# Performance work log

Hardware: AMD Instinct MI355X
Metric: run time of the kernel (lower is better)

## Reference

```python
import jax, jax.numpy as jnp
import numpy as np

N = 100000
E = 1600000
D_IN = 64
D_H = 64
D_OUT = 10
EPS_BN = 1e-5
EPS_NORM = 1e-12


def setup_inputs() -> dict:
    key = jax.random.key(0)
    ks = jax.random.split(key, 16)
    x = jax.random.normal(ks[0], (N, D_IN), dtype=jnp.float32)
    edge_index = jax.random.randint(ks[1], (2, E), 0, N, dtype=jnp.int64)
    def lin(k, fo, fi):
        s = 1.0 / np.sqrt(fi)
        return jax.random.uniform(k, (fo, fi), jnp.float32, -s, s)
    return {
        "x": x, "edge_index": edge_index,
        "Wl1": lin(ks[2], D_H, D_IN), "Wr1": lin(ks[3], D_H, D_IN), "b1": jnp.zeros((D_H,), jnp.float32),
        "g1": jnp.ones((D_H,), jnp.float32), "be1": jnp.zeros((D_H,), jnp.float32),
        "Wl2": lin(ks[4], D_H, D_H), "Wr2": lin(ks[5], D_H, D_H), "b2": jnp.zeros((D_H,), jnp.float32),
        "g2": jnp.ones((D_H,), jnp.float32), "be2": jnp.zeros((D_H,), jnp.float32),
        "Wl3": lin(ks[6], D_OUT, D_H), "Wr3": lin(ks[7], D_OUT, D_H), "b3": jnp.zeros((D_OUT,), jnp.float32),
    }


def _sage_conv(x, src, dst, Wl, Wr, b, normalize):
    # mean aggregation over incoming edges (messages flow src -> dst)
    agg = jax.ops.segment_sum(x[src], dst, num_segments=N)
    cnt = jax.ops.segment_sum(jnp.ones((src.shape[0],), x.dtype), dst, num_segments=N)
    mean = agg / jnp.clip(cnt, 1.0)[:, None]
    out = mean @ Wl.T + x @ Wr.T + b
    if normalize:
        nrm = jnp.sqrt(jnp.sum(out * out, axis=-1, keepdims=True))
        out = out / jnp.maximum(nrm, EPS_NORM)
    return out


def _batchnorm(x, gamma, beta):
    mu = jnp.mean(x, axis=0)
    var = jnp.mean((x - mu) ** 2, axis=0)  # biased var (training mode)
    return (x - mu) * jax.lax.rsqrt(var + EPS_BN) * gamma + beta


def reference(x, edge_index, Wl1, Wr1, b1, g1, be1, Wl2, Wr2, b2, g2, be2, Wl3, Wr3, b3):
    src, dst = edge_index[0], edge_index[1]
    h = _sage_conv(x, src, dst, Wl1, Wr1, b1, True)
    h = jax.nn.relu(_batchnorm(h, g1, be1))
    h = _sage_conv(h, src, dst, Wl2, Wr2, b2, True)
    h = jax.nn.relu(_batchnorm(h, g2, be2))
    h = _sage_conv(h, src, dst, Wl3, Wr3, b3, False)
    return h
```

## Files before the change

kernel.cpp:

```cpp
#include <hip/hip_runtime.h>
#include <hip/hip_bf16.h>

#define NN 100000
#define EE 1600000
#define BSZ 512
#define NBKT 196
#define CHUNK 8192
#define NCH 196

typedef short bf16x8 __attribute__((ext_vector_type(8)));
typedef float f32x4 __attribute__((ext_vector_type(4)));

__device__ inline unsigned short bf16_of(float f) {
    __hip_bfloat16 h = __float2bfloat16(f);
    return *reinterpret_cast<unsigned short*>(&h);
}
__device__ inline unsigned pack2(float a, float b) {
    return (unsigned)bf16_of(a) | ((unsigned)bf16_of(b) << 16);
}
__device__ inline float bflo(unsigned u) { return __uint_as_float(u << 16); }
__device__ inline float bfhi(unsigned u) { return __uint_as_float(u & 0xffff0000u); }


__global__ __launch_bounds__(256)
void k_ccount(const int* __restrict__ ei, int* __restrict__ ccount) {
    __shared__ int hist[NBKT];
    int tid = threadIdx.x;
    int e0 = blockIdx.x * CHUNK;
    int e1 = e0 + CHUNK; if (e1 > EE) e1 = EE;
    for (int i = tid; i < NBKT; i += 256) hist[i] = 0;
    __syncthreads();
    for (int e = e0 + tid; e < e1; e += 256)
        atomicAdd(&hist[ei[EE + e] >> 9], 1);
    __syncthreads();
    for (int i = tid; i < NBKT; i += 256)
        if (hist[i]) atomicAdd(&ccount[i], hist[i]);
}

__global__ void k_cscan(const int* __restrict__ ccount, int* __restrict__ cbase,
                        int* __restrict__ gcur) {
    __shared__ int s[256];
    int tid = threadIdx.x;
    int v = (tid < NBKT) ? ccount[tid] : 0;
    s[tid] = v;
    __syncthreads();
    for (int off = 1; off < 256; off <<= 1) {
        int t = (tid >= off) ? s[tid - off] : 0;
        __syncthreads();
        if (tid >= off) s[tid] += t;
        __syncthreads();
    }
    if (tid < NBKT) {
        int excl = s[tid] - v;
        cbase[tid] = excl;
        gcur[tid] = excl;
    }
    if (tid == NBKT - 1) cbase[NBKT] = s[tid];
}

__global__ __launch_bounds__(256)
void k_coarse(const int* __restrict__ ei, int* __restrict__ gcur, int2* __restrict__ pairs) {
    __shared__ int hist[NBKT];
    __shared__ int base[NBKT];
    __shared__ int curs[NBKT];
    int tid = threadIdx.x;
    int e0 = blockIdx.x * CHUNK;
    int e1 = e0 + CHUNK; if (e1 > EE) e1 = EE;
    for (int i = tid; i < NBKT; i += 256) hist[i] = 0;
    __syncthreads();
    for (int e = e0 + tid; e < e1; e += 256)
        atomicAdd(&hist[ei[EE + e] >> 9], 1);
    __syncthreads();
    for (int i = tid; i < NBKT; i += 256) {
        base[i] = atomicAdd(&gcur[i], hist[i]);
        curs[i] = 0;
    }
    __syncthreads();
    for (int e = e0 + tid; e < e1; e += 256) {
        int src = ei[e];
        int dst = ei[EE + e];
        int b = dst >> 9;
        int off = atomicAdd(&curs[b], 1);
        pairs[base[b] + off] = make_int2(src, dst);
    }
}

__global__ __launch_bounds__(512)
void k_fine(const int* __restrict__ cbase, const int2* __restrict__ pairs,
            int* __restrict__ rs, int* __restrict__ esrc) {
    __shared__ int deg[BSZ];
    __shared__ int s[BSZ];
    int b = blockIdx.x;
    int n0 = b * BSZ;
    int nlocal = NN - n0; if (nlocal > BSZ) nlocal = BSZ;
    int tid = threadIdx.x;
    deg[tid] = 0;
    __syncthreads();
    int e0 = cbase[b], e1 = cbase[b + 1];
    for (int e = e0 + tid; e < e1; e += 512)
        atomicAdd(&deg[pairs[e].y - n0], 1);
    __syncthreads();
    int v = deg[tid];
    s[tid] = v;
    __syncthreads();
    for (int off = 1; off < 512; off <<= 1) {
        int t = (tid >= off) ? s[tid - off] : 0;
        __syncthreads();
        if (tid >= off) s[tid] += t;
        __syncthreads();
    }
    int excl = s[tid] - v;
    if (tid < nlocal) rs[n0 + tid] = e0 + excl;
    if (b == NBKT - 1 && tid == 0) rs[NN] = EE;
    deg[tid] = e0 + excl;
    __syncthreads();
    for (int e = e0 + tid; e < e1; e += 512) {
        int2 p = pairs[e];
        int pos = atomicAdd(&deg[p.y - n0], 1);
        esrc[pos] = p.x;
    }
}

__global__ void k_tobf(const float4* __restrict__ src, ushort4* __restrict__ dst) {
    int i = blockIdx.x * 256 + threadIdx.x;
    if (i >= NN * 16) return;
    float4 v = src[i];
    dst[i] = make_ushort4(bf16_of(v.x), bf16_of(v.y), bf16_of(v.z), bf16_of(v.w));
}

__global__ void k_packW(const float* __restrict__ Wl1, const float* __restrict__ Wr1,
                        const float* __restrict__ Wl2, const float* __restrict__ Wr2,
                        unsigned short* __restrict__ w1, unsigned short* __restrict__ w2) {
    int tid = threadIdx.x;
    for (int i = tid; i < 8192; i += 256) {
        int n = i >> 7, k = i & 127;
        float v1 = (k < 64) ? Wl1[n * 64 + k] : Wr1[n * 64 + (k - 64)];
        w1[i] = bf16_of(v1);
        float v2 = (k < 64) ? Wl2[n * 64 + k] : Wr2[n * 64 + (k - 64)];
        w2[i] = bf16_of(v2);
    }
}

__global__ __launch_bounds__(256)
void k_aggbf(const unsigned short* __restrict__ xbf, const int* __restrict__ rs,
             const int* __restrict__ esrc, unsigned short* __restrict__ meanbf,
             const float* __restrict__ sc, const float* __restrict__ sh) {
    int gid = blockIdx.x * 256 + threadIdx.x;
    int node = gid >> 6;
    if (node >= NN) return;
    int lane = threadIdx.x & 63;
    int c = lane & 7;
    int slot = lane >> 3;
    int s0 = rs[node], s1 = rs[node + 1];
    const uint4* xb = (const uint4*)xbf;
    float a0 = 0.f, a1 = 0.f, a2 = 0.f, a3 = 0.f, a4 = 0.f, a5 = 0.f, a6 = 0.f, a7 = 0.f;
    if (sc) {
        float4 scl = ((const float4*)sc)[2 * c], sch = ((const float4*)sc)[2 * c + 1];
        float4 shl = ((const float4*)sh)[2 * c], shh = ((const float4*)sh)[2 * c + 1];
        for (int p = s0 + slot; p < s1; p += 8) {
            uint4 v = xb[esrc[p] * 8 + c];
            a0 += fmaxf(fmaf(bflo(v.x), scl.x, shl.x), 0.f);
            a1 += fmaxf(fmaf(bfhi(v.x), scl.y, shl.y), 0.f);
            a2 += fmaxf(fmaf(bflo(v.y), scl.z, shl.z), 0.f);
            a3 += fmaxf(fmaf(bfhi(v.y), scl.w, shl.w), 0.f);
            a4 += fmaxf(fmaf(bflo(v.z), sch.x, shh.x), 0.f);
            a5 += fmaxf(fmaf(bfhi(v.z), sch.y, shh.y), 0.f);
            a6 += fmaxf(fmaf(bflo(v.w), sch.z, shh.z), 0.f);
            a7 += fmaxf(fmaf(bfhi(v.w), sch.w, shh.w), 0.f);
        }
    } else {
        for (int p = s0 + slot; p < s1; p += 8) {
            uint4 v = xb[esrc[p] * 8 + c];
            a0 += bflo(v.x); a1 += bfhi(v.x);
            a2 += bflo(v.y); a3 += bfhi(v.y);
            a4 += bflo(v.z); a5 += bfhi(v.z);
            a6 += bflo(v.w); a7 += bfhi(v.w);
        }
    }
#pragma unroll
    for (int m = 8; m <= 32; m <<= 1) {
        a0 += __shfl_xor(a0, m, 64); a1 += __shfl_xor(a1, m, 64);
        a2 += __shfl_xor(a2, m, 64); a3 += __shfl_xor(a3, m, 64);
        a4 += __shfl_xor(a4, m, 64); a5 += __shfl_xor(a5, m, 64);
        a6 += __shfl_xor(a6, m, 64); a7 += __shfl_xor(a7, m, 64);
    }
    if (slot == 0) {
        int cnt = s1 - s0; if (cnt < 1) cnt = 1;
        float inv = 1.0f / (float)cnt;
        uint4 o;
        o.x = pack2(a0 * inv, a1 * inv);
        o.y = pack2(a2 * inv, a3 * inv);
        o.z = pack2(a4 * inv, a5 * inv);
        o.w = pack2(a6 * inv, a7 * inv);
        ((uint4*)meanbf)[node * 8 + c] = o;
    }
}

__global__ __launch_bounds__(256, 4)
void k_sagemfma(const unsigned short* __restrict__ meanbf,
                const unsigned short* __restrict__ a2bf,
                const unsigned short* __restrict__ Wbf,
                const float* __restrict__ bias,
                unsigned short* __restrict__ outbf,
                float* __restrict__ partials,
                const float* __restrict__ sc, const float* __restrict__ sh) {
    __shared__ float sblk[64];
    __shared__ float qblk[64];
    const int tid = threadIdx.x;
    const int base = blockIdx.x * 64;
    const int col = tid & 15;
    const int q   = (tid >> 4) & 3;
    const int w   = tid >> 6;

    if (tid < 64) { sblk[tid] = 0.f; qblk[tid] = 0.f; }

    int gn = base + w * 16 + col; if (gn > NN - 1) gn = NN - 1;
    const uint4* mb = (const uint4*)meanbf;
    const uint4* ab = (const uint4*)a2bf;
    const uint4* wb = (const uint4*)Wbf;

    uint4 fa0 = mb[gn * 8 + q];
    uint4 fa1 = mb[gn * 8 + 4 + q];
    uint4 fa2 = ab[gn * 8 + q];
    uint4 fa3 = ab[gn * 8 + 4 + q];
    if (sc) {
        float4 s0 = ((const float4*)sc)[q * 2],     s1 = ((const float4*)sc)[q * 2 + 1];
        float4 h0 = ((const float4*)sh)[q * 2],     h1 = ((const float4*)sh)[q * 2 + 1];
        float4 s2 = ((const float4*)sc)[8 + q * 2], s3 = ((const float4*)sc)[8 + q * 2 + 1];
        float4 h2 = ((const float4*)sh)[8 + q * 2], h3 = ((const float4*)sh)[8 + q * 2 + 1];
        fa2.x = pack2(fmaxf(fmaf(bflo(fa2.x), s0.x, h0.x), 0.f),
                      fmaxf(fmaf(bfhi(fa2.x), s0.y, h0.y), 0.f));
        fa2.y = pack2(fmaxf(fmaf(bflo(fa2.y), s0.z, h0.z), 0.f),
                      fmaxf(fmaf(bfhi(fa2.y), s0.w, h0.w), 0.f));
        fa2.z = pack2(fmaxf(fmaf(bflo(fa2.z), s1.x, h1.x), 0.f),
                      fmaxf(fmaf(bfhi(fa2.z), s1.y, h1.y), 0.f));
        fa2.w = pack2(fmaxf(fmaf(bflo(fa2.w), s1.z, h1.z), 0.f),
                      fmaxf(fmaf(bfhi(fa2.w), s1.w, h1.w), 0.f));
        fa3.x = pack2(fmaxf(fmaf(bflo(fa3.x), s2.x, h2.x), 0.f),
                      fmaxf(fmaf(bfhi(fa3.x), s2.y, h2.y), 0.f));
        fa3.y = pack2(fmaxf(fmaf(bflo(fa3.y), s2.z, h2.z), 0.f),
                      fmaxf(fmaf(bfhi(fa3.y), s2.w, h2.w), 0.f));
        fa3.z = pack2(fmaxf(fmaf(bflo(fa3.z), s3.x, h3.x), 0.f),
                      fmaxf(fmaf(bfhi(fa3.z), s3.y, h3.y), 0.f));
        fa3.w = pack2(fmaxf(fmaf(bflo(fa3.w), s3.z, h3.z), 0.f),
                      fmaxf(fmaf(bfhi(fa3.w), s3.w, h3.w), 0.f));
    }
    uint4 fa[4] = {fa0, fa1, fa2, fa3};

    f32x4 acc0 = {0.f, 0.f, 0.f, 0.f}, acc1 = acc0, acc2 = acc0, acc3 = acc0;
#pragma unroll
    for (int c = 0; c < 4; ++c) {
        uint4 b0 = wb[(0 * 16 + col) * 16 + c * 4 + q];
        uint4 b1 = wb[(1 * 16 + col) * 16 + c * 4 + q];
        uint4 b2 = wb[(2 * 16 + col) * 16 + c * 4 + q];
        uint4 b3 = wb[(3 * 16 + col) * 16 + c * 4 + q];
        bf16x8 a = *(const bf16x8*)&fa[c];
        acc0 = __builtin_amdgcn_mfma_f32_16x16x32_bf16(a, *(const bf16x8*)&b0, acc0, 0, 0, 0);
        acc1 = __builtin_amdgcn_mfma_f32_16x16x32_bf16(a, *(const bf16x8*)&b1, acc1, 0, 0, 0);
        acc2 = __builtin_amdgcn_mfma_f32_16x16x32_bf16(a, *(const bf16x8*)&b2, acc2, 0, 0, 0);
        acc3 = __builtin_amdgcn_mfma_f32_16x16x32_bf16(a, *(const bf16x8*)&b3, acc3, 0, 0, 0);
    }

    float bb0 = bias[col], bb1 = bias[16 + col], bb2 = bias[32 + col], bb3 = bias[48 + col];
    float sj0 = 0.f, sj1 = 0.f, sj2 = 0.f, sj3 = 0.f;
    float qj0 = 0.f, qj1 = 0.f, qj2 = 0.f, qj3 = 0.f;
#pragma unroll
    for (int r = 0; r < 4; ++r) {
        int go = base + w * 16 + q * 4 + r;
        float o0 = acc0[r] + bb0, o1 = acc1[r] + bb1;
        float o2 = acc2[r] + bb2, o3 = acc3[r] + bb3;
        float ssv = o0 * o0 + o1 * o1 + o2 * o2 + o3 * o3;
        ssv += __shfl_xor(ssv, 1, 64);
        ssv += __shfl_xor(ssv, 2, 64);
        ssv += __shfl_xor(ssv, 4, 64);
        ssv += __shfl_xor(ssv, 8, 64);
        float inv = 1.0f / fmaxf(sqrtf(ssv), 1e-12f);
        o0 *= inv; o1 *= inv; o2 *= inv; o3 *= inv;
        if (go < NN) {
            outbf[go * 64 + col]      = bf16_of(o0);
            outbf[go * 64 + 16 + col] = bf16_of(o1);
            outbf[go * 64 + 32 + col] = bf16_of(o2);
            outbf[go * 64 + 48 + col] = bf16_of(o3);
            sj0 += o0; sj1 += o1; sj2 += o2; sj3 += o3;
            qj0 += o0 * o0; qj1 += o1 * o1; qj2 += o2 * o2; qj3 += o3 * o3;
        }
    }
#pragma unroll
    for (int m = 16; m <= 32; m <<= 1) {
        sj0 += __shfl_xor(sj0, m, 64); sj1 += __shfl_xor(sj1, m, 64);
        sj2 += __shfl_xor(sj2, m, 64); sj3 += __shfl_xor(sj3, m, 64);
        qj0 += __shfl_xor(qj0, m, 64); qj1 += __shfl_xor(qj1, m, 64);
        qj2 += __shfl_xor(qj2, m, 64); qj3 += __shfl_xor(qj3, m, 64);
    }
    __syncthreads();
    if (q == 0) {
        atomicAdd(&sblk[col], sj0);      atomicAdd(&qblk[col], qj0);
        atomicAdd(&sblk[16 + col], sj1); atomicAdd(&qblk[16 + col], qj1);
        atomicAdd(&sblk[32 + col], sj2); atomicAdd(&qblk[32 + col], qj2);
        atomicAdd(&sblk[48 + col], sj3); atomicAdd(&qblk[48 + col], qj3);
    }
    __syncthreads();
    if (tid < 128)
        partials[blockIdx.x * 128 + tid] = (tid < 64) ? sblk[tid] : qblk[tid - 64];
}

__global__ __launch_bounds__(256)
void k_bnred(const float* __restrict__ partials, int nblk, float* __restrict__ red) {
    __shared__ float s[256];
    int tid = threadIdx.x;
    int idx = tid & 127, half = tid >> 7;
    float a0 = 0.f, a1 = 0.f, a2 = 0.f, a3 = 0.f;
    int r = blockIdx.x * 2 + half;
    for (; r + 192 < nblk; r += 256) {
        a0 += partials[r * 128 + idx];
        a1 += partials[(r + 64) * 128 + idx];
        a2 += partials[(r + 128) * 128 + idx];
        a3 += partials[(r + 192) * 128 + idx];
    }
    for (; r < nblk; r += 64) a0 += partials[r * 128 + idx];
    s[tid] = (a0 + a1) + (a2 + a3);
    __syncthreads();
    if (tid < 128) red[blockIdx.x * 128 + tid] = s[tid] + s[tid + 128];
}

__global__ void k_bnfin(const float* __restrict__ red,
                        const float* __restrict__ g, const float* __restrict__ be,
                        float* __restrict__ scale, float* __restrict__ shift) {
    __shared__ float s[256];
    int tid = threadIdx.x;
    int idx = tid & 127, half = tid >> 7;
    float a = 0.f;
#pragma unroll
    for (int r = half; r < 32; r += 2)
        a += red[r * 128 + idx];
    s[tid] = a;
    __syncthreads();
    if (tid < 128) s[tid] += s[tid + 128];
    __syncthreads();
    if (tid < 64) {
        float mu = s[tid] / (float)NN;
        float var = s[64 + tid] / (float)NN - mu * mu;
        var = fmaxf(var, 0.0f);
        float sc = g[tid] / sqrtf(var + 1e-5f);
        scale[tid] = sc;
        shift[tid] = be[tid] - mu * sc;
    }
}

__global__ __launch_bounds__(256)
void k_project(const unsigned short* __restrict__ h,
               const float* __restrict__ sc, const float* __restrict__ sh,
               const float* __restrict__ Wl, const float* __restrict__ Wr,
               const float* __restrict__ bias,
               float* __restrict__ zl, float* __restrict__ zr) {
    __shared__ float Alds[64 * 128];
    __shared__ float Wlds[64 * 32];
    const int tid = threadIdx.x;
    const int base = blockIdx.x * 128;

#pragma unroll
    for (int i = 0; i < 8; ++i) {
        int idx = i * 256 + tid;
        int f = idx & 31, k = idx >> 5;
        float v = 0.0f;
        if (f < 16) { if (f < 10) v = Wl[f * 64 + k]; }
        else        { if (f - 16 < 10) v = Wr[(f - 16) * 64 + k]; }
        Wlds[k * 32 + f] = v;
    }
    {
        const uint4* h4 = (const uint4*)h;
        const float4* sc4p = (const float4*)sc;
        const float4* sh4p = (const float4*)sh;
#pragma unroll
        for (int i = 0; i < 4; ++i) {
            int idx = i * 256 + tid;
            int node = idx & 127, cb = idx >> 7;
            int gn = base + node; if (gn > NN - 1) gn = NN - 1;
            uint4 u = h4[gn * 8 + cb];
            float4 sA = sc4p[cb * 2], sB = sc4p[cb * 2 + 1];
            float4 hA = sh4p[cb * 2], hB = sh4p[cb * 2 + 1];
            int k0 = cb * 8;
            Alds[(k0 + 0) * 128 + node] = fmaxf(fmaf(bflo(u.x), sA.x, hA.x), 0.f);
            Alds[(k0 + 1) * 128 + node] = fmaxf(fmaf(bfhi(u.x), sA.y, hA.y), 0.f);
            Alds[(k0 + 2) * 128 + node] = fmaxf(fmaf(bflo(u.y), sA.z, hA.z), 0.f);
            Alds[(k0 + 3) * 128 + node] = fmaxf(fmaf(bfhi(u.y), sA.w, hA.w), 0.f);
            Alds[(k0 + 4) * 128 + node] = fmaxf(fmaf(bflo(u.z), sB.x, hB.x), 0.f);
            Alds[(k0 + 5) * 128 + node] = fmaxf(fmaf(bfhi(u.z), sB.y, hB.y), 0.f);
            Alds[(k0 + 6) * 128 + node] = fmaxf(fmaf(bflo(u.w), sB.z, hB.z), 0.f);
            Alds[(k0 + 7) * 128 + node] = fmaxf(fmaf(bfhi(u.w), sB.w, hB.w), 0.f);
        }
    }
    __syncthreads();

    const int fg = tid & 7;
    const int ng = tid >> 3;

    float acc[4][4] = {};
#pragma unroll 4
    for (int k = 0; k < 64; ++k) {
        const float4 a = *(const float4*)(Alds + k * 128 + (ng << 2));
        const float4 w = *(const float4*)(Wlds + k * 32 + (fg << 2));
        const float av[4] = {a.x, a.y, a.z, a.w};
        const float wv[4] = {w.x, w.y, w.z, w.w};
#pragma unroll
        for (int i = 0; i < 4; ++i)
#pragma unroll
            for (int j = 0; j < 4; ++j)
                acc[i][j] = fmaf(av[i], wv[j], acc[i][j]);
    }

    if (fg == 3 || fg == 7) return;
    float4* dst = (fg < 4) ? (float4*)zl : (float4*)zr;
    int fq = (fg < 4) ? fg : fg - 4;
    float bx = 0.f, by = 0.f, bz = 0.f, bw = 0.f;
    if (fg >= 4) {
        int f0 = fq * 4;
        bx = (f0 + 0 < 10) ? bias[f0 + 0] : 0.f;
        by = (f0 + 1 < 10) ? bias[f0 + 1] : 0.f;
        bz = (f0 + 2 < 10) ? bias[f0 + 2] : 0.f;
        bw = (f0 + 3 < 10) ? bias[f0 + 3] : 0.f;
    }
#pragma unroll
    for (int i = 0; i < 4; ++i) {
        int gn = base + (ng << 2) + i;
        if (gn < NN)
            dst[gn * 3 + fq] = make_float4(acc[i][0] + bx, acc[i][1] + by,
                                           acc[i][2] + bz, acc[i][3] + bw);
    }
}

__global__ __launch_bounds__(256)
void k_agg10(const int* __restrict__ rs, const int* __restrict__ esrc,
             const float* __restrict__ zl, const float* __restrict__ zr,
             float* __restrict__ out) {
    int gid = blockIdx.x * 256 + threadIdx.x;
    unsigned node = (unsigned)gid / 3u;
    int j = gid - (int)node * 3;
    if (node >= NN) return;
    int s0 = rs[node], s1 = rs[node + 1];
    const float4* zl4 = (const float4*)zl;
    float4 acc = make_float4(0.f, 0.f, 0.f, 0.f);
    for (int p = s0; p < s1; ++p) {
        float4 v = zl4[esrc[p] * 3 + j];
        acc.x += v.x; acc.y += v.y; acc.z += v.z; acc.w += v.w;
    }
    int cnt = s1 - s0; if (cnt < 1) cnt = 1;
    float inv = 1.0f / (float)cnt;
    float4 r = ((const float4*)zr)[node * 3 + j];
    r.x = fmaf(acc.x, inv, r.x); r.y = fmaf(acc.y, inv, r.y);
    r.z = fmaf(acc.z, inv, r.z); r.w = fmaf(acc.w, inv, r.w);
    float2* o2 = (float2*)(out + (size_t)node * 10);
    if (j < 2) {
        o2[j * 2 + 0] = make_float2(r.x, r.y);
        o2[j * 2 + 1] = make_float2(r.z, r.w);
    } else {
        o2[4] = make_float2(r.x, r.y);
    }
}


extern "C" void kernel_launch(void* const* d_in, const int* in_sizes, int n_in,
                              void* d_out, int out_size, void* d_ws, size_t ws_size,
                              hipStream_t stream) {
    const float* x   = (const float*)d_in[0];
    const int*   ei  = (const int*)d_in[1];
    const float* Wl1 = (const float*)d_in[2];
    const float* Wr1 = (const float*)d_in[3];
    const float* b1  = (const float*)d_in[4];
    const float* g1  = (const float*)d_in[5];
    const float* be1 = (const float*)d_in[6];
    const float* Wl2 = (const float*)d_in[7];
    const float* Wr2 = (const float*)d_in[8];
    const float* b2  = (const float*)d_in[9];
    const float* g2  = (const float*)d_in[10];
    const float* be2 = (const float*)d_in[11];
    const float* Wl3 = (const float*)d_in[12];
    const float* Wr3 = (const float*)d_in[13];
    const float* b3  = (const float*)d_in[14];
    float* out = (float*)d_out;

    char* w = (char*)d_ws;
    auto alloc = [&](size_t bytes) -> void* {
        void* p = (void*)w;
        w += (bytes + 255) & ~(size_t)255;
        return p;
    };
    int*   ccount = (int*)alloc(256 * 4);
    int*   cbase  = (int*)alloc(256 * 4);
    int*   gcur   = (int*)alloc(256 * 4);
    int*   rs     = (int*)alloc((size_t)(NN + 1) * 4);
    int*   esrc   = (int*)alloc((size_t)EE * 4);
    float* scratch= (float*)alloc((size_t)NN * 64 * 4);
    unsigned short* xbf    = (unsigned short*)alloc((size_t)NN * 64 * 2);
    unsigned short* h1bf   = (unsigned short*)alloc((size_t)NN * 64 * 2);
    unsigned short* meanbf = (unsigned short*)alloc((size_t)NN * 64 * 2);
    unsigned short* wbf1   = (unsigned short*)alloc(8192 * 2);
    unsigned short* wbf2   = (unsigned short*)alloc(8192 * 2);
    float* partials = (float*)alloc((size_t)1563 * 128 * 4);
    float* red    = (float*)alloc(32 * 128 * 4);
    float* scsh   = (float*)alloc(256 * 4);
    int2*  pairs  = (int2*)scratch;
    float* zl     = scratch;
    float* zr     = scratch + (size_t)NN * 12;

    hipMemsetAsync(ccount, 0, 256 * 4, stream);

    k_ccount<<<NCH, 256, 0, stream>>>(ei, ccount);
    k_cscan<<<1, 256, 0, stream>>>(ccount, cbase, gcur);
    k_coarse<<<NCH, 256, 0, stream>>>(ei, gcur, pairs);
    k_fine<<<NBKT, 512, 0, stream>>>(cbase, pairs, rs, esrc);
    k_tobf<<<(NN * 16 + 255) / 256, 256, 0, stream>>>((const float4*)x, (ushort4*)xbf);
    k_packW<<<1, 256, 0, stream>>>(Wl1, Wr1, Wl2, Wr2, wbf1, wbf2);

    const int aggBlocks  = (NN * 64) / 256;
    const int sageBlocks = (NN + 63) / 64;
    const int projBlocks = (NN + 127) / 128;
    const int a10Blocks  = (NN * 3 + 255) / 256;

    k_aggbf<<<aggBlocks, 256, 0, stream>>>(xbf, rs, esrc, meanbf, nullptr, nullptr);
    k_sagemfma<<<sageBlocks, 256, 0, stream>>>(meanbf, xbf, wbf1, b1, h1bf,
                                               partials, nullptr, nullptr);
    k_bnred<<<32, 256, 0, stream>>>(partials, sageBlocks, red);
    k_bnfin<<<1, 256, 0, stream>>>(red, g1, be1, scsh + 0, scsh + 64);

    k_aggbf<<<aggBlocks, 256, 0, stream>>>(h1bf, rs, esrc, meanbf, scsh + 0, scsh + 64);
    k_sagemfma<<<sageBlocks, 256, 0, stream>>>(meanbf, h1bf, wbf2, b2, xbf,
                                               partials, scsh + 0, scsh + 64);
    k_bnred<<<32, 256, 0, stream>>>(partials, sageBlocks, red);
    k_bnfin<<<1, 256, 0, stream>>>(red, g2, be2, scsh + 128, scsh + 192);

    k_project<<<projBlocks, 256, 0, stream>>>(xbf, scsh + 128, scsh + 192,
                                              Wl3, Wr3, b3, zl, zr);
    k_agg10<<<a10Blocks, 256, 0, stream>>>(rs, esrc, zl, zr, out);
}
```

Before: 355.6 us.

## Pack CSR build pairs into single ints and unroll gather loops for more loads in flight

Edge pairs in the coarse/fine CSR build are packed into one 32-bit int (src<<9 | local dst), halving the intermediate pair traffic. The gather loops in the bf16 aggregation and the final 10-wide aggregation are unrolled by 2 and 4 so more independent gathers are outstanding per thread. A launch-bounds occupancy hint is added to the aggregation kernel. The packing relies on src fitting in 23 bits, which holds for N=100000.

```diff
diff --git a/kernel.cpp b/kernel.cpp
--- a/kernel.cpp
+++ b/kernel.cpp
@@ -59,7 +59,7 @@
 }
 
 __global__ __launch_bounds__(256)
-void k_coarse(const int* __restrict__ ei, int* __restrict__ gcur, int2* __restrict__ pairs) {
+void k_coarse(const int* __restrict__ ei, int* __restrict__ gcur, int* __restrict__ pairs) {
     __shared__ int hist[NBKT];
     __shared__ int base[NBKT];
     __shared__ int curs[NBKT];
@@ -81,12 +81,12 @@
         int dst = ei[EE + e];
         int b = dst >> 9;
         int off = atomicAdd(&curs[b], 1);
-        pairs[base[b] + off] = make_int2(src, dst);
+        pairs[base[b] + off] = (src << 9) | (dst & 511);
     }
 }
 
 __global__ __launch_bounds__(512)
-void k_fine(const int* __restrict__ cbase, const int2* __restrict__ pairs,
+void k_fine(const int* __restrict__ cbase, const int* __restrict__ pairs,
             int* __restrict__ rs, int* __restrict__ esrc) {
     __shared__ int deg[BSZ];
     __shared__ int s[BSZ];
@@ -98,7 +98,7 @@
     __syncthreads();
     int e0 = cbase[b], e1 = cbase[b + 1];
     for (int e = e0 + tid; e < e1; e += 512)
-        atomicAdd(&deg[pairs[e].y - n0], 1);
+        atomicAdd(&deg[pairs[e] & 511], 1);
     __syncthreads();
     int v = deg[tid];
     s[tid] = v;
@@ -115,9 +115,9 @@
     deg[tid] = e0 + excl;
     __syncthreads();
     for (int e = e0 + tid; e < e1; e += 512) {
-        int2 p = pairs[e];
-        int pos = atomicAdd(&deg[p.y - n0], 1);
-        esrc[pos] = p.x;
+        int pk = pairs[e];
+        int pos = atomicAdd(&deg[pk & 511], 1);
+        esrc[pos] = pk >> 9;
     }
 }
 
@@ -141,7 +141,7 @@
     }
 }
 
-__global__ __launch_bounds__(256)
+__global__ __launch_bounds__(256, 8)
 void k_aggbf(const unsigned short* __restrict__ xbf, const int* __restrict__ rs,
              const int* __restrict__ esrc, unsigned short* __restrict__ meanbf,
              const float* __restrict__ sc, const float* __restrict__ sh) {
@@ -157,24 +157,54 @@
     if (sc) {
         float4 scl = ((const float4*)sc)[2 * c], sch = ((const float4*)sc)[2 * c + 1];
         float4 shl = ((const float4*)sh)[2 * c], shh = ((const float4*)sh)[2 * c + 1];
-        for (int p = s0 + slot; p < s1; p += 8) {
-            uint4 v = xb[esrc[p] * 8 + c];
-            a0 += fmaxf(fmaf(bflo(v.x), scl.x, shl.x), 0.f);
-            a1 += fmaxf(fmaf(bfhi(v.x), scl.y, shl.y), 0.f);
-            a2 += fmaxf(fmaf(bflo(v.y), scl.z, shl.z), 0.f);
-            a3 += fmaxf(fmaf(bfhi(v.y), scl.w, shl.w), 0.f);
-            a4 += fmaxf(fmaf(bflo(v.z), sch.x, shh.x), 0.f);
-            a5 += fmaxf(fmaf(bfhi(v.z), sch.y, shh.y), 0.f);
-            a6 += fmaxf(fmaf(bflo(v.w), sch.z, shh.z), 0.f);
-            a7 += fmaxf(fmaf(bfhi(v.w), sch.w, shh.w), 0.f);
+        int p = s0 + slot;
+        for (; p + 8 < s1; p += 16) {
+            uint4 va = xb[esrc[p] * 8 + c];
+            uint4 vb = xb[esrc[p + 8] * 8 + c];
+            a0 += fmaxf(fmaf(bflo(va.x), scl.x, shl.x), 0.f);
+            a1 += fmaxf(fmaf(bfhi(va.x), scl.y, shl.y), 0.f);
+            a2 += fmaxf(fmaf(bflo(va.y), scl.z, shl.z), 0.f);
+            a3 += fmaxf(fmaf(bfhi(va.y), scl.w, shl.w), 0.f);
+            a4 += fmaxf(fmaf(bflo(va.z), sch.x, shh.x), 0.f);
+            a5 += fmaxf(fmaf(bfhi(va.z), sch.y, shh.y), 0.f);
+            a6 += fmaxf(fmaf(bflo(va.w), sch.z, shh.z), 0.f);
+            a7 += fmaxf(fmaf(bfhi(va.w), sch.w, shh.w), 0.f);
+            a0 += fmaxf(fmaf(bflo(vb.x), scl.x, shl.x), 0.f);
+            a1 += fmaxf(fmaf(bfhi(vb.x), scl.y, shl.y), 0.f);
+            a2 += fmaxf(fmaf(bflo(vb.y), scl.z, shl.z), 0.f);
+            a3 += fmaxf(fmaf(bfhi(vb.y), scl.w, shl.w), 0.f);
+            a4 += fmaxf(fmaf(bflo(vb.z), sch.x, shh.x), 0.f);
+            a5 += fmaxf(fmaf(bfhi(vb.z), sch.y, shh.y), 0.f);
+            a6 += fmaxf(fmaf(bflo(vb.w), sch.z, shh.z), 0.f);
+            a7 += fmaxf(fmaf(bfhi(vb.w), sch.w, shh.w), 0.f);
+        }
+        if (p < s1) {
+            uint4 va = xb[esrc[p] * 8 + c];
+            a0 += fmaxf(fmaf(bflo(va.x), scl.x, shl.x), 0.f);
+            a1 += fmaxf(fmaf(bfhi(va.x), scl.y, shl.y), 0.f);
+            a2 += fmaxf(fmaf(bflo(va.y), scl.z, shl.z), 0.f);
+            a3 += fmaxf(fmaf(bfhi(va.y), scl.w, shl.w), 0.f);
+            a4 += fmaxf(fmaf(bflo(va.z), sch.x, shh.x), 0.f);
+            a5 += fmaxf(fmaf(bfhi(va.z), sch.y, shh.y), 0.f);
+            a6 += fmaxf(fmaf(bflo(va.w), sch.z, shh.z), 0.f);
+            a7 += fmaxf(fmaf(bfhi(va.w), sch.w, shh.w), 0.f);
         }
     } else {
-        for (int p = s0 + slot; p < s1; p += 8) {
-            uint4 v = xb[esrc[p] * 8 + c];
-            a0 += bflo(v.x); a1 += bfhi(v.x);
-            a2 += bflo(v.y); a3 += bfhi(v.y);
-            a4 += bflo(v.z); a5 += bfhi(v.z);
-            a6 += bflo(v.w); a7 += bfhi(v.w);
+        int p = s0 + slot;
+        for (; p + 8 < s1; p += 16) {
+            uint4 va = xb[esrc[p] * 8 + c];
+            uint4 vb = xb[esrc[p + 8] * 8 + c];
+            a0 += bflo(va.x) + bflo(vb.x); a1 += bfhi(va.x) + bfhi(vb.x);
+            a2 += bflo(va.y) + bflo(vb.y); a3 += bfhi(va.y) + bfhi(vb.y);
+            a4 += bflo(va.z) + bflo(vb.z); a5 += bfhi(va.z) + bfhi(vb.z);
+            a6 += bflo(va.w) + bflo(vb.w); a7 += bfhi(va.w) + bfhi(vb.w);
+        }
+        if (p < s1) {
+            uint4 va = xb[esrc[p] * 8 + c];
+            a0 += bflo(va.x); a1 += bfhi(va.x);
+            a2 += bflo(va.y); a3 += bfhi(va.y);
+            a4 += bflo(va.z); a5 += bfhi(va.z);
+            a6 += bflo(va.w); a7 += bfhi(va.w);
         }
     }
 #pragma unroll
@@ -440,7 +470,18 @@
     int s0 = rs[node], s1 = rs[node + 1];
     const float4* zl4 = (const float4*)zl;
     float4 acc = make_float4(0.f, 0.f, 0.f, 0.f);
-    for (int p = s0; p < s1; ++p) {
+    int p = s0;
+    for (; p + 3 < s1; p += 4) {
+        float4 v0 = zl4[esrc[p] * 3 + j];
+        float4 v1 = zl4[esrc[p + 1] * 3 + j];
+        float4 v2 = zl4[esrc[p + 2] * 3 + j];
+        float4 v3 = zl4[esrc[p + 3] * 3 + j];
+        acc.x += (v0.x + v1.x) + (v2.x + v3.x);
+        acc.y += (v0.y + v1.y) + (v2.y + v3.y);
+        acc.z += (v0.z + v1.z) + (v2.z + v3.z);
+        acc.w += (v0.w + v1.w) + (v2.w + v3.w);
+    }
+    for (; p < s1; ++p) {
         float4 v = zl4[esrc[p] * 3 + j];
         acc.x += v.x; acc.y += v.y; acc.z += v.z; acc.w += v.w;
     }
@@ -499,7 +540,7 @@
     float* partials = (float*)alloc((size_t)1563 * 128 * 4);
     float* red    = (float*)alloc(32 * 128 * 4);
     float* scsh   = (float*)alloc(256 * 4);
-    int2*  pairs  = (int2*)scratch;
+    int*   pairs  = (int*)scratch;
     float* zl     = scratch;
     float* zr     = scratch + (size_t)NN * 12;
 
```

Result: faster. 339.9 us (-4.4%).
